# Kernel tuning notes

Hardware: AMD Instinct MI355X
Metric: run time of the kernel (lower is better)

The kernel has to match this reference:

```python
import jax, jax.numpy as jnp
import numpy as np

V = 100000
E = 1600000
BN_EPS = 1e-5


def spmm(edge_index, vals, X):
    # X: (V, Cin, B); sparse L @ X via scatter-add. y[r] += w * X[c]
    rows, cols = edge_index[0], edge_index[1]
    return jnp.zeros_like(X).at[rows].add(vals[:, None, None] * X[cols])


def cheb_conv(x, edge_index, vals, w, b=None):
    # x: (B, Cin, V), w: (K, Cin, Cout) -> (B, Cout, V)
    K = w.shape[0]
    x0 = jnp.transpose(x, (2, 1, 0))  # (V, Cin, B)
    xs = [x0]
    if K > 1:
        x1 = spmm(edge_index, vals, x0)
        xs.append(x1)
        for _ in range(2, K):
            x2 = 2.0 * spmm(edge_index, vals, x1) - x0
            xs.append(x2)
            x0, x1 = x1, x2
    xk = jnp.stack(xs)  # (K, V, Cin, B)
    out = jnp.einsum('kvcb,kco->bov', xk, w)
    if b is not None:
        out = out + b[None, :, None]
    return out


def batch_norm(x, g, b):
    # training-mode BatchNorm1d on (B, C, V): stats over (B, V), biased var
    m = jnp.mean(x, axis=(0, 2), keepdims=True)
    v = jnp.var(x, axis=(0, 2), keepdims=True)
    return g[None, :, None] * (x - m) * jax.lax.rsqrt(v + BN_EPS) + b[None, :, None]


def setup_inputs() -> dict:
    key = jax.random.key(0)
    ks = jax.random.split(key, 8)
    x = jax.random.normal(ks[0], (4, 32, V), dtype=jnp.float32)
    edge_index = jax.random.randint(ks[1], (2, E), 0, V, dtype=jnp.int32)
    # small values keep the K=4 Chebyshev recursion well-scaled
    lap_vals = 0.1 * jax.random.normal(ks[2], (E,), dtype=jnp.float32)
    def w(k, K, cin, cout):
        s = 1.0 / np.sqrt(K * cin)
        return s * jax.random.normal(k, (K, cin, cout), dtype=jnp.float32)
    return {
        'x': x, 'edge_index': edge_index, 'lap_vals': lap_vals,
        'in_bn_g': jnp.ones((32,), jnp.float32), 'in_bn_b': jnp.zeros((32,), jnp.float32),
        'in_w': w(ks[3], 4, 32, 64), 'in_b': jnp.zeros((64,), jnp.float32),
        'h0_bn_g': jnp.ones((64,), jnp.float32), 'h0_bn_b': jnp.zeros((64,), jnp.float32),
        'h0_w': w(ks[4], 4, 64, 64), 'h0_b': jnp.zeros((64,), jnp.float32),
        'h1_bn_g': jnp.ones((64,), jnp.float32), 'h1_bn_b': jnp.zeros((64,), jnp.float32),
        'h1_w': w(ks[5], 4, 64, 32), 'h1_b': jnp.zeros((32,), jnp.float32),
    }


def reference(x, edge_index, lap_vals, in_bn_g, in_bn_b, in_w, in_b,
              h0_bn_g, h0_bn_b, h0_w, h0_b, h1_bn_g, h1_bn_b, h1_w, h1_b):
    xn = batch_norm(x, in_bn_g, in_bn_b)
    out = cheb_conv(xn, edge_index, lap_vals, in_w, in_b)
    # hidden layer 0
    out = jax.nn.relu(out)
    out = batch_norm(out, h0_bn_g, h0_bn_b)
    out = cheb_conv(out, edge_index, lap_vals, h0_w, h0_b)
    # hidden layer 1
    out = jax.nn.relu(out)
    out = batch_norm(out, h1_bn_g, h1_bn_b)
    out = cheb_conv(out, edge_index, lap_vals, h1_w, h1_b)
    # in_channels == out_channels -> Identity shortcut on the BN'ed input
    return jax.nn.relu(out + xn)
```

## Files before the change

kernel.cpp:

```cpp
#include <hip/hip_runtime.h>
#include <cstdint>
#include <cstddef>

#define VN 100000
#define EN 1600000
static constexpr float BN_EPS_F = 1e-5f;
static constexpr float INV_N = 1.0f / 400000.0f;

using short8 = __attribute__((ext_vector_type(8))) short;
using f32x4  = __attribute__((ext_vector_type(4))) float;

__device__ __forceinline__ float bf_lo(unsigned int p) {
  return __builtin_bit_cast(float, p << 16);
}
__device__ __forceinline__ float bf_hi(unsigned int p) {
  return __builtin_bit_cast(float, p & 0xffff0000u);
}
__device__ __forceinline__ float bf1(unsigned short u) {
  return __builtin_bit_cast(float, ((unsigned int)u) << 16);
}
__device__ __forceinline__ unsigned short f2bf(float f) {
  unsigned int x = __builtin_bit_cast(unsigned int, f);
  x += 0x7fffu + ((x >> 16) & 1u);
  return (unsigned short)(x >> 16);
}
__device__ __forceinline__ unsigned int pack2(float a, float b) {
  return (unsigned int)f2bf(a) | ((unsigned int)f2bf(b) << 16);
}

__global__ __launch_bounds__(256) void stats_x_kernel(const float* __restrict__ x,
                                                      float* __restrict__ stats) {
  const int p = blockIdx.x & 127;
  const int chunk = blockIdx.x >> 7;
  const int c = p & 31, b = p >> 5;
  const float* base = x + ((size_t)b * 32 + c) * VN + chunk * 12500;
  float s = 0.f, s2 = 0.f;
  for (int i = threadIdx.x; i < 12500; i += 256) {
    float v = base[i];
    s += v; s2 += v * v;
  }
  __shared__ float r1[256], r2[256];
  r1[threadIdx.x] = s; r2[threadIdx.x] = s2;
  __syncthreads();
  for (int off = 128; off > 0; off >>= 1) {
    if (threadIdx.x < off) {
      r1[threadIdx.x] += r1[threadIdx.x + off];
      r2[threadIdx.x] += r2[threadIdx.x + off];
    }
    __syncthreads();
  }
  if (threadIdx.x == 0) {
    atomicAdd(&stats[c], r1[0]);
    atomicAdd(&stats[64 + c], r2[0]);
  }
}

__global__ void finalize_stats_kernel(float* __restrict__ stats,
                                      const float* __restrict__ g,
                                      const float* __restrict__ beta, int C) {
  int c = threadIdx.x;
  if (c < C) {
    float m = stats[c] * INV_N;
    float var = stats[64 + c] * INV_N - m * m;
    float sc = g[c] * rsqrtf(var + BN_EPS_F);
    stats[128 + c] = sc;
    stats[192 + c] = beta[c] - m * sc;
  }
}

__global__ __launch_bounds__(128) void bn_transpose_kernel(const float* __restrict__ x,
                                                           const float* __restrict__ stats,
                                                           unsigned short* __restrict__ xn) {
  const int tid = threadIdx.x;
  const int b = tid >> 5, c = tid & 31;
  const int v0 = blockIdx.x * 64;
  const float sc = stats[128 + c], sh = stats[192 + c];
  const float* src = x + ((size_t)b * 32 + c) * VN;
  for (int i = 0; i < 64; i++) {
    int v = v0 + i;
    if (v < VN) xn[(size_t)v * 128 + tid] = f2bf(sc * src[v] + sh);
  }
}

__global__ __launch_bounds__(256) void pack_wb_kernel(const float* __restrict__ W,
                                                      unsigned short* __restrict__ Wb,
                                                      int Cin, int Cout) {
  const int i = blockIdx.x * 256 + threadIdx.x;
  const int KC = Cin >> 5, T = Cout >> 4;
  const int tot = 4 * KC * T * 512;
  if (i >= tot) return;
  const int j = i & 7;
  const int l = (i >> 3) & 63;
  const int rem = i >> 9;
  const int t = rem % T;
  const int kc = (rem / T) % KC;
  const int k = rem / (T * KC);
  const int c = kc * 32 + (l >> 4) * 8 + j;
  const int o = t * 16 + (l & 15);
  Wb[i] = f2bf(W[((size_t)k * Cin + c) * Cout + o]);
}

__global__ __launch_bounds__(256) void hist_kernel(const int* __restrict__ rows,
                                                   int* __restrict__ cnt) {
  int i = blockIdx.x * blockDim.x + threadIdx.x;
  const int stride = gridDim.x * blockDim.x;
  for (; i < EN; i += stride) atomicAdd(&cnt[rows[i]], 1);
}

__global__ __launch_bounds__(256) void scan1_kernel(const int* __restrict__ cnt,
                                                    int* __restrict__ rp,
                                                    int* __restrict__ chunkSums) {
  __shared__ int sh[256];
  const int t = threadIdx.x;
  const int base = blockIdx.x * 2048 + t * 8;
  int vals[8]; int tot = 0;
#pragma unroll
  for (int i = 0; i < 8; i++) {
    int idx = base + i;
    int v = (idx < VN) ? cnt[idx] : 0;
    vals[i] = v; tot += v;
  }
  sh[t] = tot;
  __syncthreads();
  for (int off = 1; off < 256; off <<= 1) {
    int v = (t >= off) ? sh[t - off] : 0;
    __syncthreads();
    sh[t] += v;
    __syncthreads();
  }
  int run = sh[t] - tot;
#pragma unroll
  for (int i = 0; i < 8; i++) {
    int idx = base + i;
    if (idx < VN) rp[idx] = run;
    run += vals[i];
  }
  if (t == 255) chunkSums[blockIdx.x] = sh[255];
}

__global__ void scan2_kernel(const int* __restrict__ chunkSums,
                             int* __restrict__ chunkOff,
                             int* __restrict__ rp, int nChunks) {
  if (threadIdx.x == 0 && blockIdx.x == 0) {
    int off = 0;
    for (int j = 0; j < nChunks; j++) { chunkOff[j] = off; off += chunkSums[j]; }
    rp[VN] = off;
  }
}

__global__ __launch_bounds__(256) void scan3_kernel(int* __restrict__ rp,
                                                    const int* __restrict__ chunkOff,
                                                    int* __restrict__ fill) {
  int i = blockIdx.x * 256 + threadIdx.x;
  if (i < VN) {
    int v = rp[i] + chunkOff[i >> 11];
    rp[i] = v;
    fill[i] = v;
  }
}

__global__ __launch_bounds__(256) void fill_kernel(const int* __restrict__ rows,
                                                   const int* __restrict__ cols,
                                                   const float* __restrict__ lap,
                                                   int* __restrict__ fill,
                                                   int* __restrict__ cols_s,
                                                   float* __restrict__ vals_s) {
  int i = blockIdx.x * blockDim.x + threadIdx.x;
  const int stride = gridDim.x * blockDim.x;
  for (; i < EN; i += stride) {
    int r = rows[i];
    int pos = atomicAdd(&fill[r], 1);
    cols_s[pos] = cols[i];
    vals_s[pos] = lap[i];
  }
}

template <int EPL, bool CHEB>
__global__ __launch_bounds__(256, 8) void spmm_kernel(const int* __restrict__ rp,
                                                   const int* __restrict__ cs,
                                                   const float* __restrict__ vs,
                                                   const unsigned short* __restrict__ X, int XS,
                                                   const unsigned short* __restrict__ P, int PS,
                                                   unsigned short* __restrict__ Y, int YS) {
  const int lane = threadIdx.x & 63;
  const int row = blockIdx.x * 4 + (threadIdx.x >> 6);
  const int start = rp[row], end = rp[row + 1];
  float acc[EPL];
#pragma unroll
  for (int j = 0; j < EPL; j++) acc[j] = 0.f;
  int e = start;
  for (; e + 4 <= end; e += 4) {
    const int c0 = cs[e], c1 = cs[e + 1], c2 = cs[e + 2], c3 = cs[e + 3];
    const float w0 = vs[e], w1 = vs[e + 1], w2 = vs[e + 2], w3 = vs[e + 3];
    if constexpr (EPL == 4) {
      const uint2 q0 = *reinterpret_cast<const uint2*>(X + (size_t)c0 * XS + lane * 4);
      const uint2 q1 = *reinterpret_cast<const uint2*>(X + (size_t)c1 * XS + lane * 4);
      const uint2 q2 = *reinterpret_cast<const uint2*>(X + (size_t)c2 * XS + lane * 4);
      const uint2 q3 = *reinterpret_cast<const uint2*>(X + (size_t)c3 * XS + lane * 4);
      acc[0] += w0 * bf_lo(q0.x) + w1 * bf_lo(q1.x) + w2 * bf_lo(q2.x) + w3 * bf_lo(q3.x);
      acc[1] += w0 * bf_hi(q0.x) + w1 * bf_hi(q1.x) + w2 * bf_hi(q2.x) + w3 * bf_hi(q3.x);
      acc[2] += w0 * bf_lo(q0.y) + w1 * bf_lo(q1.y) + w2 * bf_lo(q2.y) + w3 * bf_lo(q3.y);
      acc[3] += w0 * bf_hi(q0.y) + w1 * bf_hi(q1.y) + w2 * bf_hi(q2.y) + w3 * bf_hi(q3.y);
    } else {
      const unsigned int q0 = *reinterpret_cast<const unsigned int*>(X + (size_t)c0 * XS + lane * 2);
      const unsigned int q1 = *reinterpret_cast<const unsigned int*>(X + (size_t)c1 * XS + lane * 2);
      const unsigned int q2 = *reinterpret_cast<const unsigned int*>(X + (size_t)c2 * XS + lane * 2);
      const unsigned int q3 = *reinterpret_cast<const unsigned int*>(X + (size_t)c3 * XS + lane * 2);
      acc[0] += w0 * bf_lo(q0) + w1 * bf_lo(q1) + w2 * bf_lo(q2) + w3 * bf_lo(q3);
      acc[1] += w0 * bf_hi(q0) + w1 * bf_hi(q1) + w2 * bf_hi(q2) + w3 * bf_hi(q3);
    }
  }
  for (; e < end; e++) {
    const int c0 = cs[e];
    const float w0 = vs[e];
    if constexpr (EPL == 4) {
      const uint2 q0 = *reinterpret_cast<const uint2*>(X + (size_t)c0 * XS + lane * 4);
      acc[0] += w0 * bf_lo(q0.x);
      acc[1] += w0 * bf_hi(q0.x);
      acc[2] += w0 * bf_lo(q0.y);
      acc[3] += w0 * bf_hi(q0.y);
    } else {
      const unsigned int q0 = *reinterpret_cast<const unsigned int*>(X + (size_t)c0 * XS + lane * 2);
      acc[0] += w0 * bf_lo(q0);
      acc[1] += w0 * bf_hi(q0);
    }
  }
  if constexpr (EPL == 4) {
    if constexpr (CHEB) {
      const uint2 p = *reinterpret_cast<const uint2*>(P + (size_t)row * PS + lane * 4);
      acc[0] = 2.f * acc[0] - bf_lo(p.x);
      acc[1] = 2.f * acc[1] - bf_hi(p.x);
      acc[2] = 2.f * acc[2] - bf_lo(p.y);
      acc[3] = 2.f * acc[3] - bf_hi(p.y);
    }
    uint2 r;
    r.x = pack2(acc[0], acc[1]);
    r.y = pack2(acc[2], acc[3]);
    *reinterpret_cast<uint2*>(Y + (size_t)row * YS + lane * 4) = r;
  } else {
    if constexpr (CHEB) {
      const unsigned int p = *reinterpret_cast<const unsigned int*>(P + (size_t)row * PS + lane * 2);
      acc[0] = 2.f * acc[0] - bf_lo(p);
      acc[1] = 2.f * acc[1] - bf_hi(p);
    }
    *reinterpret_cast<unsigned int*>(Y + (size_t)row * YS + lane * 2) = pack2(acc[0], acc[1]);
  }
}

template <int Cin, int Cout, int X0S>
__global__ __launch_bounds__(256, 8) void fused_cheb_kernel(const int* __restrict__ rp,
                                                         const int* __restrict__ cs,
                                                         const float* __restrict__ vs,
                                                         const unsigned short* __restrict__ X0,
                                                         unsigned short* __restrict__ A,
                                                         const unsigned short* __restrict__ B,
                                                         const unsigned short* __restrict__ Wb,
                                                         const float* __restrict__ Bias) {
  constexpr int EPL = Cin * 4 / 64;
  constexpr int ROWSH = Cin * 4;
  __shared__ unsigned short t3s[4 * ROWSH];
  const int lane = threadIdx.x & 63;
  const int wv = threadIdx.x >> 6;
  const int row0 = blockIdx.x * 4;
  const int row = row0 + wv;

  float g[EPL];
#pragma unroll
  for (int j = 0; j < EPL; j++) g[j] = 0.f;
  const int start = rp[row], end = rp[row + 1];
  int e = start;
  for (; e + 4 <= end; e += 4) {
    const int c0 = cs[e], c1 = cs[e + 1], c2 = cs[e + 2], c3 = cs[e + 3];
    const float w0 = vs[e], w1 = vs[e + 1], w2 = vs[e + 2], w3 = vs[e + 3];
    if constexpr (EPL == 4) {
      const uint2 q0 = *reinterpret_cast<const uint2*>(B + (size_t)c0 * 256 + lane * 4);
      const uint2 q1 = *reinterpret_cast<const uint2*>(B + (size_t)c1 * 256 + lane * 4);
      const uint2 q2 = *reinterpret_cast<const uint2*>(B + (size_t)c2 * 256 + lane * 4);
      const uint2 q3 = *reinterpret_cast<const uint2*>(B + (size_t)c3 * 256 + lane * 4);
      g[0] += w0 * bf_lo(q0.x) + w1 * bf_lo(q1.x) + w2 * bf_lo(q2.x) + w3 * bf_lo(q3.x);
      g[1] += w0 * bf_hi(q0.x) + w1 * bf_hi(q1.x) + w2 * bf_hi(q2.x) + w3 * bf_hi(q3.x);
      g[2] += w0 * bf_lo(q0.y) + w1 * bf_lo(q1.y) + w2 * bf_lo(q2.y) + w3 * bf_lo(q3.y);
      g[3] += w0 * bf_hi(q0.y) + w1 * bf_hi(q1.y) + w2 * bf_hi(q2.y) + w3 * bf_hi(q3.y);
    } else {
      const unsigned int q0 = *reinterpret_cast<const unsigned int*>(B + (size_t)c0 * 256 + lane * 2);
      const unsigned int q1 = *reinterpret_cast<const unsigned int*>(B + (size_t)c1 * 256 + lane * 2);
      const unsigned int q2 = *reinterpret_cast<const unsigned int*>(B + (size_t)c2 * 256 + lane * 2);
      const unsigned int q3 = *reinterpret_cast<const unsigned int*>(B + (size_t)c3 * 256 + lane * 2);
      g[0] += w0 * bf_lo(q0) + w1 * bf_lo(q1) + w2 * bf_lo(q2) + w3 * bf_lo(q3);
      g[1] += w0 * bf_hi(q0) + w1 * bf_hi(q1) + w2 * bf_hi(q2) + w3 * bf_hi(q3);
    }
  }
  for (; e < end; e++) {
    const int c0 = cs[e];
    const float w0 = vs[e];
    if constexpr (EPL == 4) {
      const uint2 q0 = *reinterpret_cast<const uint2*>(B + (size_t)c0 * 256 + lane * 4);
      g[0] += w0 * bf_lo(q0.x);
      g[1] += w0 * bf_hi(q0.x);
      g[2] += w0 * bf_lo(q0.y);
      g[3] += w0 * bf_hi(q0.y);
    } else {
      const unsigned int q0 = *reinterpret_cast<const unsigned int*>(B + (size_t)c0 * 256 + lane * 2);
      g[0] += w0 * bf_lo(q0);
      g[1] += w0 * bf_hi(q0);
    }
  }
  {
    unsigned int* tw = reinterpret_cast<unsigned int*>(t3s + wv * ROWSH);
    if constexpr (EPL == 4) {
      const uint2 p = *reinterpret_cast<const uint2*>(A + (size_t)row * 256 + lane * 4);
      tw[lane * 2]     = pack2(2.f * g[0] - bf_lo(p.x), 2.f * g[1] - bf_hi(p.x));
      tw[lane * 2 + 1] = pack2(2.f * g[2] - bf_lo(p.y), 2.f * g[3] - bf_hi(p.y));
    } else {
      const unsigned int p = *reinterpret_cast<const unsigned int*>(A + (size_t)row * 256 + lane * 2);
      tw[lane] = pack2(2.f * g[0] - bf_lo(p), 2.f * g[1] - bf_hi(p));
    }
  }
  __syncthreads();

  constexpr int KC = Cin / 32;
  constexpr int T = Cout / 16;
  const int col = lane & 15, quad = lane >> 4;
  const int t = wv % T;
  const int ar = col >> 2, ab = col & 3;

  const unsigned short* xap[3];
  xap[0] = X0 + (size_t)(row0 + ar) * X0S + ab * Cin + quad * 8;
  xap[1] = A  + (size_t)(row0 + ar) * 256 + ab * Cin + quad * 8;
  xap[2] = B  + (size_t)(row0 + ar) * 256 + ab * Cin + quad * 8;
  const unsigned short* wb = Wb + (size_t)t * 512 + lane * 8;

  f32x4 acc = {0.f, 0.f, 0.f, 0.f};
#pragma unroll
  for (int k = 0; k < 3; k++) {
#pragma unroll
    for (int kc = 0; kc < KC; kc++) {
      const short8 af = *reinterpret_cast<const short8*>(xap[k] + kc * 32);
      const short8 bf = *reinterpret_cast<const short8*>(wb + (size_t)(k * KC + kc) * T * 512);
      acc = __builtin_amdgcn_mfma_f32_16x16x32_bf16(af, bf, acc, 0, 0, 0);
    }
  }
#pragma unroll
  for (int kc = 0; kc < KC; kc++) {
    const short8 af = *reinterpret_cast<const short8*>(&t3s[ar * ROWSH + ab * Cin + kc * 32 + quad * 8]);
    const short8 bf = *reinterpret_cast<const short8*>(wb + (size_t)(3 * KC + kc) * T * 512);
    acc = __builtin_amdgcn_mfma_f32_16x16x32_bf16(af, bf, acc, 0, 0, 0);
  }
  __syncthreads();

  if (T == 4 || wv < 2) {
    const int og = t * 16 + col;
    const float bs = Bias[og];
#pragma unroll
    for (int r = 0; r < 4; r++) {
      A[(size_t)(row0 + quad) * 256 + r * Cout + og] = f2bf(acc[r] + bs);
    }
  }
}

__global__ __launch_bounds__(256) void stats_out_kernel(const unsigned short* __restrict__ SRC,
                                                        float* __restrict__ stats) {
  const int tid = threadIdx.x;
  const int per = (VN + gridDim.x - 1) / gridDim.x;
  const int v0 = blockIdx.x * per;
  const int v1 = (v0 + per < VN) ? (v0 + per) : VN;
  float s = 0.f, s2 = 0.f;
  for (int v = v0; v < v1; v++) {
    float val = bf1(SRC[(size_t)v * 256 + tid]);
    val = fmaxf(val, 0.f);
    s += val; s2 += val * val;
  }
  __shared__ float r1[256], r2[256];
  r1[tid] = s; r2[tid] = s2;
  __syncthreads();
  if (tid < 64) {
    float a = r1[tid] + r1[tid + 64] + r1[tid + 128] + r1[tid + 192];
    float b = r2[tid] + r2[tid + 64] + r2[tid + 128] + r2[tid + 192];
    atomicAdd(&stats[tid], a);
    atomicAdd(&stats[64 + tid], b);
  }
}

__global__ __launch_bounds__(256) void bn_relu_kernel(const unsigned short* __restrict__ SRC,
                                                      const float* __restrict__ stats,
                                                      unsigned short* __restrict__ DST) {
  const int i = blockIdx.x * 256 + threadIdx.x;
  const int w = i & 63;
  const int o0 = (w & 15) * 4;
  const float4 sc4 = *reinterpret_cast<const float4*>(stats + 128 + o0);
  const float4 sh4 = *reinterpret_cast<const float4*>(stats + 192 + o0);
  const uint2 q = reinterpret_cast<const uint2*>(SRC)[i];
  float a = fmaxf(bf_lo(q.x), 0.f);
  float b = fmaxf(bf_hi(q.x), 0.f);
  float c = fmaxf(bf_lo(q.y), 0.f);
  float d = fmaxf(bf_hi(q.y), 0.f);
  uint2 r;
  r.x = pack2(a * sc4.x + sh4.x, b * sc4.y + sh4.y);
  r.y = pack2(c * sc4.z + sh4.z, d * sc4.w + sh4.w);
  reinterpret_cast<uint2*>(DST)[i] = r;
}

__global__ __launch_bounds__(256) void final_kernel(const unsigned short* __restrict__ SRC,
                                                    const unsigned short* __restrict__ xn,
                                                    float* __restrict__ out) {
  const int lane = threadIdx.x & 63;
  const int grp = threadIdx.x >> 6;
  const int v = blockIdx.x * 64 + lane;
  if (v >= VN) return;
  for (int ob = grp; ob < 128; ob += 4) {
    float val = bf1(SRC[(size_t)v * 256 + ob]) + bf1(xn[(size_t)v * 128 + ob]);
    val = fmaxf(val, 0.f);
    out[(size_t)ob * VN + v] = val;
  }
}

static constexpr size_t align_up(size_t x) { return (x + 255) & ~(size_t)255; }
static constexpr size_t OFF_RP    = 0;
static constexpr size_t OFF_FILL  = align_up(OFF_RP + (size_t)(VN + 1) * 4);
static constexpr size_t OFF_CHS   = align_up(OFF_FILL + (size_t)VN * 4);
static constexpr size_t OFF_CHO   = align_up(OFF_CHS + 256);
static constexpr size_t OFF_STATS = align_up(OFF_CHO + 256);
static constexpr size_t OFF_WP    = align_up(OFF_STATS + 1024);
static constexpr size_t OFF_CS    = align_up(OFF_WP + 32768 * 2);
static constexpr size_t OFF_VS    = align_up(OFF_CS + (size_t)EN * 4);
static constexpr size_t OFF_XN    = align_up(OFF_VS + (size_t)EN * 4);
static constexpr size_t OFF_XL    = align_up(OFF_XN + (size_t)VN * 128 * 2);
static constexpr size_t OFF_A     = align_up(OFF_XL + (size_t)VN * 256 * 2);
static constexpr size_t OFF_B     = align_up(OFF_A + (size_t)VN * 256 * 2);
static constexpr size_t OFF_END   = OFF_B + (size_t)VN * 256 * 2;

extern "C" void kernel_launch(void* const* d_in, const int* in_sizes, int n_in,
                              void* d_out, int out_size, void* d_ws, size_t ws_size,
                              hipStream_t stream) {
  if (ws_size < OFF_END) return;

  const float* x       = (const float*)d_in[0];
  const int*   rows    = (const int*)d_in[1];
  const int*   cols    = rows + EN;
  const float* lap     = (const float*)d_in[2];
  const float* in_bn_g = (const float*)d_in[3];
  const float* in_bn_b = (const float*)d_in[4];
  const float* in_w    = (const float*)d_in[5];
  const float* in_b    = (const float*)d_in[6];
  const float* h0_bn_g = (const float*)d_in[7];
  const float* h0_bn_b = (const float*)d_in[8];
  const float* h0_w    = (const float*)d_in[9];
  const float* h0_b    = (const float*)d_in[10];
  const float* h1_bn_g = (const float*)d_in[11];
  const float* h1_bn_b = (const float*)d_in[12];
  const float* h1_w    = (const float*)d_in[13];
  const float* h1_b    = (const float*)d_in[14];
  float* outp = (float*)d_out;

  char* ws = (char*)d_ws;
  int*   rp     = (int*)(ws + OFF_RP);
  int*   fill   = (int*)(ws + OFF_FILL);
  int*   chS    = (int*)(ws + OFF_CHS);
  int*   chO    = (int*)(ws + OFF_CHO);
  float* stats  = (float*)(ws + OFF_STATS);
  unsigned short* wbIn = (unsigned short*)(ws + OFF_WP);
  unsigned short* wbH0 = wbIn + 8192;
  unsigned short* wbH1 = wbH0 + 16384;
  int*   cs     = (int*)(ws + OFF_CS);
  float* vs     = (float*)(ws + OFF_VS);
  unsigned short* xn = (unsigned short*)(ws + OFF_XN);
  unsigned short* XL = (unsigned short*)(ws + OFF_XL);
  unsigned short* A  = (unsigned short*)(ws + OFF_A);
  unsigned short* B  = (unsigned short*)(ws + OFF_B);

  const int nChunks = (VN + 2047) / 2048;

  pack_wb_kernel<<<32, 256, 0, stream>>>(in_w, wbIn, 32, 64);
  pack_wb_kernel<<<64, 256, 0, stream>>>(h0_w, wbH0, 64, 64);
  pack_wb_kernel<<<32, 256, 0, stream>>>(h1_w, wbH1, 64, 32);

  hipMemsetAsync(stats, 0, 1024, stream);
  stats_x_kernel<<<1024, 256, 0, stream>>>(x, stats);
  finalize_stats_kernel<<<1, 64, 0, stream>>>(stats, in_bn_g, in_bn_b, 32);
  bn_transpose_kernel<<<1563, 128, 0, stream>>>(x, stats, xn);

  hipMemsetAsync(fill, 0, (size_t)VN * 4, stream);
  hist_kernel<<<2048, 256, 0, stream>>>(rows, fill);
  scan1_kernel<<<nChunks, 256, 0, stream>>>(fill, rp, chS);
  scan2_kernel<<<1, 64, 0, stream>>>(chS, chO, rp, nChunks);
  scan3_kernel<<<(VN + 255) / 256, 256, 0, stream>>>(rp, chO, fill);
  fill_kernel<<<2048, 256, 0, stream>>>(rows, cols, lap, fill, cs, vs);

  spmm_kernel<2, false><<<VN / 4, 256, 0, stream>>>(rp, cs, vs, xn, 128, nullptr, 0, A, 256);
  spmm_kernel<2, true ><<<VN / 4, 256, 0, stream>>>(rp, cs, vs, A, 256, xn, 128, B, 256);
  fused_cheb_kernel<32, 64, 128><<<VN / 4, 256, 0, stream>>>(rp, cs, vs, xn, A, B, wbIn, in_b);
  hipMemsetAsync(stats, 0, 1024, stream);
  stats_out_kernel<<<256, 256, 0, stream>>>(A, stats);
  finalize_stats_kernel<<<1, 64, 0, stream>>>(stats, h0_bn_g, h0_bn_b, 64);
  bn_relu_kernel<<<VN * 64 / 256, 256, 0, stream>>>(A, stats, XL);

  spmm_kernel<4, false><<<VN / 4, 256, 0, stream>>>(rp, cs, vs, XL, 256, nullptr, 0, A, 256);
  spmm_kernel<4, true ><<<VN / 4, 256, 0, stream>>>(rp, cs, vs, A, 256, XL, 256, B, 256);
  fused_cheb_kernel<64, 64, 256><<<VN / 4, 256, 0, stream>>>(rp, cs, vs, XL, A, B, wbH0, h0_b);
  hipMemsetAsync(stats, 0, 1024, stream);
  stats_out_kernel<<<256, 256, 0, stream>>>(A, stats);
  finalize_stats_kernel<<<1, 64, 0, stream>>>(stats, h1_bn_g, h1_bn_b, 64);
  bn_relu_kernel<<<VN * 64 / 256, 256, 0, stream>>>(A, stats, XL);

  spmm_kernel<4, false><<<VN / 4, 256, 0, stream>>>(rp, cs, vs, XL, 256, nullptr, 0, A, 256);
  spmm_kernel<4, true ><<<VN / 4, 256, 0, stream>>>(rp, cs, vs, A, 256, XL, 256, B, 256);
  fused_cheb_kernel<64, 32, 256><<<VN / 4, 256, 0, stream>>>(rp, cs, vs, XL, A, B, wbH1, h1_b);

  final_kernel<<<1563, 256, 0, stream>>>(A, xn, outp);
}
```

Measured before the change: 1.801 ms.

## Split 64-channel SpMM into two half-width passes with 8-way unrolled gathers

The SpMM kernel now always handles 128 bf16 values per row (two per lane). The 64-channel layers launch it twice with a column offset instead of gathering 256-wide rows. Each pass touches a smaller gathered working set, which may fit better in L2/MALL, and the inner loop issues 8 independent gathers with predicated tails for more memory-level parallelism. The cost is reading the CSR index and value arrays twice and launching more kernels.

```diff
diff --git a/kernel.cpp b/kernel.cpp
--- a/kernel.cpp
+++ b/kernel.cpp
@@ -175,76 +175,46 @@
   }
 }
 
-template <int EPL, bool CHEB>
+template <bool CHEB>
 __global__ __launch_bounds__(256, 8) void spmm_kernel(const int* __restrict__ rp,
-                                                   const int* __restrict__ cs,
-                                                   const float* __restrict__ vs,
-                                                   const unsigned short* __restrict__ X, int XS,
-                                                   const unsigned short* __restrict__ P, int PS,
-                                                   unsigned short* __restrict__ Y, int YS) {
+                                                      const int* __restrict__ cs,
+                                                      const float* __restrict__ vs,
+                                                      const unsigned short* __restrict__ X, int XS,
+                                                      const unsigned short* __restrict__ P, int PS,
+                                                      unsigned short* __restrict__ Y, int YS,
+                                                      int soff) {
   const int lane = threadIdx.x & 63;
   const int row = blockIdx.x * 4 + (threadIdx.x >> 6);
   const int start = rp[row], end = rp[row + 1];
-  float acc[EPL];
-#pragma unroll
-  for (int j = 0; j < EPL; j++) acc[j] = 0.f;
-  int e = start;
-  for (; e + 4 <= end; e += 4) {
-    const int c0 = cs[e], c1 = cs[e + 1], c2 = cs[e + 2], c3 = cs[e + 3];
-    const float w0 = vs[e], w1 = vs[e + 1], w2 = vs[e + 2], w3 = vs[e + 3];
-    if constexpr (EPL == 4) {
-      const uint2 q0 = *reinterpret_cast<const uint2*>(X + (size_t)c0 * XS + lane * 4);
-      const uint2 q1 = *reinterpret_cast<const uint2*>(X + (size_t)c1 * XS + lane * 4);
-      const uint2 q2 = *reinterpret_cast<const uint2*>(X + (size_t)c2 * XS + lane * 4);
-      const uint2 q3 = *reinterpret_cast<const uint2*>(X + (size_t)c3 * XS + lane * 4);
-      acc[0] += w0 * bf_lo(q0.x) + w1 * bf_lo(q1.x) + w2 * bf_lo(q2.x) + w3 * bf_lo(q3.x);
-      acc[1] += w0 * bf_hi(q0.x) + w1 * bf_hi(q1.x) + w2 * bf_hi(q2.x) + w3 * bf_hi(q3.x);
-      acc[2] += w0 * bf_lo(q0.y) + w1 * bf_lo(q1.y) + w2 * bf_lo(q2.y) + w3 * bf_lo(q3.y);
-      acc[3] += w0 * bf_hi(q0.y) + w1 * bf_hi(q1.y) + w2 * bf_hi(q2.y) + w3 * bf_hi(q3.y);
-    } else {
-      const unsigned int q0 = *reinterpret_cast<const unsigned int*>(X + (size_t)c0 * XS + lane * 2);
-      const unsigned int q1 = *reinterpret_cast<const unsigned int*>(X + (size_t)c1 * XS + lane * 2);
-      const unsigned int q2 = *reinterpret_cast<const unsigned int*>(X + (size_t)c2 * XS + lane * 2);
-      const unsigned int q3 = *reinterpret_cast<const unsigned int*>(X + (size_t)c3 * XS + lane * 2);
-      acc[0] += w0 * bf_lo(q0) + w1 * bf_lo(q1) + w2 * bf_lo(q2) + w3 * bf_lo(q3);
-      acc[1] += w0 * bf_hi(q0) + w1 * bf_hi(q1) + w2 * bf_hi(q2) + w3 * bf_hi(q3);
-    }
-  }
-  for (; e < end; e++) {
-    const int c0 = cs[e];
-    const float w0 = vs[e];
-    if constexpr (EPL == 4) {
-      const uint2 q0 = *reinterpret_cast<const uint2*>(X + (size_t)c0 * XS + lane * 4);
-      acc[0] += w0 * bf_lo(q0.x);
-      acc[1] += w0 * bf_hi(q0.x);
-      acc[2] += w0 * bf_lo(q0.y);
-      acc[3] += w0 * bf_hi(q0.y);
-    } else {
-      const unsigned int q0 = *reinterpret_cast<const unsigned int*>(X + (size_t)c0 * XS + lane * 2);
-      acc[0] += w0 * bf_lo(q0);
-      acc[1] += w0 * bf_hi(q0);
-    }
-  }
-  if constexpr (EPL == 4) {
-    if constexpr (CHEB) {
-      const uint2 p = *reinterpret_cast<const uint2*>(P + (size_t)row * PS + lane * 4);
-      acc[0] = 2.f * acc[0] - bf_lo(p.x);
-      acc[1] = 2.f * acc[1] - bf_hi(p.x);
-      acc[2] = 2.f * acc[2] - bf_lo(p.y);
-      acc[3] = 2.f * acc[3] - bf_hi(p.y);
-    }
-    uint2 r;
-    r.x = pack2(acc[0], acc[1]);
-    r.y = pack2(acc[2], acc[3]);
-    *reinterpret_cast<uint2*>(Y + (size_t)row * YS + lane * 4) = r;
-  } else {
-    if constexpr (CHEB) {
-      const unsigned int p = *reinterpret_cast<const unsigned int*>(P + (size_t)row * PS + lane * 2);
-      acc[0] = 2.f * acc[0] - bf_lo(p);
-      acc[1] = 2.f * acc[1] - bf_hi(p);
-    }
-    *reinterpret_cast<unsigned int*>(Y + (size_t)row * YS + lane * 2) = pack2(acc[0], acc[1]);
-  }
+  float a0 = 0.f, a1 = 0.f;
+  if (start < end) {
+    for (int e0 = start; e0 < end; e0 += 8) {
+      int c[8]; float w[8];
+#pragma unroll
+      for (int i = 0; i < 8; i++) {
+        const int e = e0 + i;
+        const int ee = (e < end) ? e : (end - 1);
+        c[i] = cs[ee];
+        w[i] = (e < end) ? vs[ee] : 0.f;
+      }
+      unsigned int q[8];
+#pragma unroll
+      for (int i = 0; i < 8; i++) {
+        q[i] = *reinterpret_cast<const unsigned int*>(X + (size_t)c[i] * XS + soff + lane * 2);
+      }
+#pragma unroll
+      for (int i = 0; i < 8; i++) {
+        a0 += w[i] * bf_lo(q[i]);
+        a1 += w[i] * bf_hi(q[i]);
+      }
+    }
+  }
+  if constexpr (CHEB) {
+    const unsigned int p = *reinterpret_cast<const unsigned int*>(P + (size_t)row * PS + soff + lane * 2);
+    a0 = 2.f * a0 - bf_lo(p);
+    a1 = 2.f * a1 - bf_hi(p);
+  }
+  *reinterpret_cast<unsigned int*>(Y + (size_t)row * YS + soff + lane * 2) = pack2(a0, a1);
 }
 
 template <int Cin, int Cout, int X0S>
@@ -486,25 +456,31 @@
   scan3_kernel<<<(VN + 255) / 256, 256, 0, stream>>>(rp, chO, fill);
   fill_kernel<<<2048, 256, 0, stream>>>(rows, cols, lap, fill, cs, vs);
 
-  spmm_kernel<2, false><<<VN / 4, 256, 0, stream>>>(rp, cs, vs, xn, 128, nullptr, 0, A, 256);
-  spmm_kernel<2, true ><<<VN / 4, 256, 0, stream>>>(rp, cs, vs, A, 256, xn, 128, B, 256);
-  fused_cheb_kernel<32, 64, 128><<<VN / 4, 256, 0, stream>>>(rp, cs, vs, xn, A, B, wbIn, in_b);
+  const int G = VN / 4;
+
+  spmm_kernel<false><<<G, 256, 0, stream>>>(rp, cs, vs, xn, 128, nullptr, 0, A, 256, 0);
+  spmm_kernel<true ><<<G, 256, 0, stream>>>(rp, cs, vs, A, 256, xn, 128, B, 256, 0);
+  fused_cheb_kernel<32, 64, 128><<<G, 256, 0, stream>>>(rp, cs, vs, xn, A, B, wbIn, in_b);
   hipMemsetAsync(stats, 0, 1024, stream);
   stats_out_kernel<<<256, 256, 0, stream>>>(A, stats);
   finalize_stats_kernel<<<1, 64, 0, stream>>>(stats, h0_bn_g, h0_bn_b, 64);
   bn_relu_kernel<<<VN * 64 / 256, 256, 0, stream>>>(A, stats, XL);
 
-  spmm_kernel<4, false><<<VN / 4, 256, 0, stream>>>(rp, cs, vs, XL, 256, nullptr, 0, A, 256);
-  spmm_kernel<4, true ><<<VN / 4, 256, 0, stream>>>(rp, cs, vs, A, 256, XL, 256, B, 256);
-  fused_cheb_kernel<64, 64, 256><<<VN / 4, 256, 0, stream>>>(rp, cs, vs, XL, A, B, wbH0, h0_b);
+  spmm_kernel<false><<<G, 256, 0, stream>>>(rp, cs, vs, XL, 256, nullptr, 0, A, 256, 0);
+  spmm_kernel<false><<<G, 256, 0, stream>>>(rp, cs, vs, XL, 256, nullptr, 0, A, 256, 128);
+  spmm_kernel<true ><<<G, 256, 0, stream>>>(rp, cs, vs, A, 256, XL, 256, B, 256, 0);
+  spmm_kernel<true ><<<G, 256, 0, stream>>>(rp, cs, vs, A, 256, XL, 256, B, 256, 128);
+  fused_cheb_kernel<64, 64, 256><<<G, 256, 0, stream>>>(rp, cs, vs, XL, A, B, wbH0, h0_b);
   hipMemsetAsync(stats, 0, 1024, stream);
   stats_out_kernel<<<256, 256, 0, stream>>>(A, stats);
   finalize_stats_kernel<<<1, 64, 0, stream>>>(stats, h1_bn_g, h1_bn_b, 64);
   bn_relu_kernel<<<VN * 64 / 256, 256, 0, stream>>>(A, stats, XL);
 
-  spmm_kernel<4, false><<<VN / 4, 256, 0, stream>>>(rp, cs, vs, XL, 256, nullptr, 0, A, 256);
-  spmm_kernel<4, true ><<<VN / 4, 256, 0, stream>>>(rp, cs, vs, A, 256, XL, 256, B, 256);
-  fused_cheb_kernel<64, 32, 256><<<VN / 4, 256, 0, stream>>>(rp, cs, vs, XL, A, B, wbH1, h1_b);
+  spmm_kernel<false><<<G, 256, 0, stream>>>(rp, cs, vs, XL, 256, nullptr, 0, A, 256, 0);
+  spmm_kernel<false><<<G, 256, 0, stream>>>(rp, cs, vs, XL, 256, nullptr, 0, A, 256, 128);
+  spmm_kernel<true ><<<G, 256, 0, stream>>>(rp, cs, vs, A, 256, XL, 256, B, 256, 0);
+  spmm_kernel<true ><<<G, 256, 0, stream>>>(rp, cs, vs, A, 256, XL, 256, B, 256, 128);
+  fused_cheb_kernel<64, 32, 256><<<G, 256, 0, stream>>>(rp, cs, vs, XL, A, B, wbH1, h1_b);
 
   final_kernel<<<1563, 256, 0, stream>>>(A, xn, outp);
 }
```

Measured after the change: 1.837 ms. Within noise of the previous version (+2.0%).
